# Performance work log

Measured on AMD Instinct MI355X. Metric: run time of the kernel, lower is better.

## Reference

```python
import jax, jax.numpy as jnp
import numpy as np
from jax.scipy.special import logsumexp

DIM_N, DIM_E, DIM_U = 64, 128, 64
MID, A = 32, 16
N_PER, B = 12, 128  # 128 fully-connected graphs of 12 nodes


def _lin_params(k, fin, fout):
    k1, k2 = jax.random.split(k)
    lim = 1.0 / np.sqrt(fin)
    W = jax.random.uniform(k1, (fin, fout), minval=-lim, maxval=lim)
    b = jax.random.uniform(k2, (fout,), minval=-lim, maxval=lim)
    return W, b


def setup_inputs() -> dict:
    key = jax.random.key(0)
    ks = jax.random.split(key, 12)
    # fully connected directed graph (no self loops), per component
    s, d = np.meshgrid(np.arange(N_PER), np.arange(N_PER), indexing='ij')
    m = s != d
    s1, d1 = s[m].astype(np.int64), d[m].astype(np.int64)
    Epg = s1.size  # 132
    M = np.zeros((N_PER, N_PER), np.int64)
    M[s1, d1] = np.arange(Epg)
    rev1 = M[d1, s1]
    noff = (np.arange(B, dtype=np.int64) * N_PER)[:, None]
    eoff = (np.arange(B, dtype=np.int64) * Epg)[:, None]
    src = jnp.asarray((s1[None] + noff).reshape(-1))
    dst = jnp.asarray((d1[None] + noff).reshape(-1))
    idx_revs = jnp.asarray((rev1[None] + eoff).reshape(-1))
    E, Nt = B * Epg, B * N_PER
    edge_feats = jax.random.normal(ks[0], (E, DIM_E))
    node_feats = jax.random.normal(ks[1], (Nt, DIM_N))
    graph_feats = jax.random.normal(ks[2], (B, DIM_U))
    edge_feat_reflected = edge_feats[idx_revs]
    u = jax.random.uniform(ks[3], (E, 2), minval=1e-6, maxval=1.0)
    gumbel_noise = -jnp.log(-jnp.log(u))
    W_jf, b_jf = _lin_params(ks[4], DIM_E + DIM_U, A * MID)
    W_if, b_if = _lin_params(ks[5], DIM_N + DIM_U, A)
    W_ju, b_ju = _lin_params(ks[6], DIM_E + DIM_U, A * MID)
    W_iu, b_iu = _lin_params(ks[7], DIM_N + DIM_U, A)
    W_fl, b_fl = _lin_params(ks[8], DIM_E + DIM_U, MID)
    W_cls, b_cls = _lin_params(ks[9], MID, 2)
    return dict(edge_feats=edge_feats, node_feats=node_feats, graph_feats=graph_feats,
                edge_feat_reflected=edge_feat_reflected, src=src, dst=dst, idx_revs=idx_revs,
                gumbel_noise=gumbel_noise, W_jf=W_jf, b_jf=b_jf, W_if=W_if, b_if=b_if,
                W_ju=W_ju, b_ju=b_ju, W_iu=W_iu, b_iu=b_iu, W_fl=W_fl, b_fl=b_fl,
                W_cls=W_cls, b_cls=b_cls)


def reference(edge_feats, node_feats, graph_feats, edge_feat_reflected, src, dst, idx_revs,
              gumbel_noise, W_jf, b_jf, W_if, b_if, W_ju, b_ju, W_iu, b_iu,
              W_fl, b_fl, W_cls, b_cls):
    Bn = graph_feats.shape[0]
    Nt = node_feats.shape[0]
    E = edge_feats.shape[0]
    npg = Nt // Bn          # nodes per graph == number of BP iterations
    epg = E // Bn
    a = b_if.shape[0]       # num_acts
    mid = W_cls.shape[0]    # mid_pair

    # broadcast graph-level features to edges / nodes
    u_e = jnp.repeat(graph_feats, epg, axis=0)   # [E, du]
    u_n = jnp.repeat(graph_feats, npg, axis=0)   # [Nt, du]

    xe = jnp.concatenate([edge_feats, u_e], axis=-1)
    xer = jnp.concatenate([edge_feat_reflected, u_e], axis=-1)
    xn = jnp.concatenate([node_feats, u_n], axis=-1)

    indiv_factor = xn @ W_if + b_if      # [Nt, A]
    indiv_util = xn @ W_iu + b_iu        # [Nt, A]

    fc = (xe @ W_jf + b_jf).reshape(E, a, mid)
    fcr = (xer @ W_jf + b_jf).reshape(E, a, mid)
    factor_vals = jnp.einsum('eam,ebm->eab', fc, fcr)   # [E, A, A]
    uc = (xe @ W_ju + b_ju).reshape(E, a, mid)
    ucr = (xer @ W_ju + b_ju).reshape(E, a, mid)
    util_vals = jnp.einsum('eam,ebm->eab', uc, ucr)     # [E, A, A]

    # hard gumbel-softmax edge gating; noise shared with reverse edge
    flag_repr = (xe @ W_fl + b_fl) * (xer @ W_fl + b_fl)
    logits = flag_repr @ W_cls + b_cls                  # [E, 2]
    eid = jnp.arange(E)
    noise = gumbel_noise[jnp.minimum(eid, idx_revs)]
    y_soft = jax.nn.softmax(logits + noise, axis=-1)
    y_hard = jax.nn.one_hot(jnp.argmax(y_soft, axis=-1), 2, dtype=y_soft.dtype)
    flags = y_soft + jax.lax.stop_gradient(y_hard - y_soft)
    flag0 = flags[:, 0][:, None]                        # [E, 1]

    fvT = factor_vals.transpose(0, 2, 1)
    uvT = util_vals.transpose(0, 2, 1)
    if_src, if_dst = indiv_factor[src], indiv_factor[dst]
    iu_src, iu_dst = indiv_util[src], indiv_util[dst]

    def step(carry, _):
        mm_n, um_n, msg_e, rmsg_e, umsg_e, rumsg_e = carry
        agg = mm_n[src] - rmsg_e + if_src                      # [E, A]
        m = factor_vals + agg[:, None, :]                      # [E, A, A]
        m_sum = jax.nn.log_softmax(logsumexp(m, axis=-1), axis=-1)
        new_msg = m_sum * flag0
        agg_rev = mm_n[dst] - msg_e + if_dst
        m_rev = fvT + agg_rev[:, None, :]
        m_rev_sum = jax.nn.log_softmax(logsumexp(m_rev, axis=-1), axis=-1)
        new_rmsg = m_rev_sum * flag0
        util = um_n[src] - rumsg_e + iu_src
        new_umsg = ((util_vals + util[:, None, :]) * jax.nn.softmax(m, axis=-1)).sum(-1) * flag0
        rev_util = um_n[dst] - umsg_e + iu_dst
        new_rumsg = ((uvT + rev_util[:, None, :]) * jax.nn.softmax(m_rev, axis=-1)).sum(-1) * flag0
        new_mm_n = jax.ops.segment_sum(new_msg, dst, num_segments=Nt)
        new_um_n = jax.ops.segment_sum(new_umsg, dst, num_segments=Nt)
        return (new_mm_n, new_um_n, new_msg, new_rmsg, new_umsg, new_rumsg), None

    zn = jnp.zeros((Nt, a), edge_feats.dtype)
    ze = jnp.zeros((E, a), edge_feats.dtype)
    carry0 = (zn, zn, ze, ze, ze, ze)
    (mm_n, um_n, _, _, _, _), _ = jax.lax.scan(step, carry0, None, length=npg)

    node0 = jnp.arange(Bn) * npg
    return (um_n + indiv_util)[node0]   # [B, A]
```

## Files before the change

kernel.cpp:

```cpp
#include <hip/hip_runtime.h>
#include <hip/hip_bf16.h>

typedef unsigned short ushort_t;
typedef __bf16 bf16x8 __attribute__((ext_vector_type(8)));
typedef float f32x4 __attribute__((ext_vector_type(4)));

#define E_TOT 16896
#define NT    1536
#define BGR   128
#define NPG   12
#define EPG   132
#define KD    192
#define KDE   128
#define KD2   384
#define NJ    512
#define NCAN  8448

#if defined(__has_builtin)
#  if __has_builtin(__builtin_amdgcn_global_load_lds)
#    define HAS_GLL 1
#  else
#    define HAS_GLL 0
#  endif
#else
#  define HAS_GLL 0
#endif

#if HAS_GLL
__device__ __forceinline__ void gll16(const ushort_t* g, ushort_t* s) {
    __builtin_amdgcn_global_load_lds(
        (const __attribute__((address_space(1))) unsigned int*)g,
        (__attribute__((address_space(3))) unsigned int*)s, 16, 0, 0);
}
#endif

__device__ __forceinline__ float b2f(ushort_t u) {
    union { float f; unsigned int i; } c; c.i = ((unsigned int)u) << 16; return c.f;
}
__device__ __forceinline__ ushort_t f2b(float f) {
    union { float f; unsigned int i; } c; c.f = f;
    unsigned int i = c.i;
    unsigned int r = (i + 0x7FFFu + ((i >> 16) & 1u)) >> 16;
    return (ushort_t)r;
}
__device__ __forceinline__ int rev_local(int i) {
    int s = i / 11;
    int p = i - 11 * s;
    int d = p + (p >= s ? 1 : 0);
    return d * 11 + (s < d ? s : s - 1);
}

__global__ __launch_bounds__(256) void prep_kernel(
    const float* __restrict__ Wjf, const float* __restrict__ Wju,
    const float* __restrict__ ef,  const float* __restrict__ gf,
    const float* __restrict__ bjf, const float* __restrict__ bju,
    const float* __restrict__ nf,
    const float* __restrict__ Wif, const float* __restrict__ bif,
    const float* __restrict__ Wiu, const float* __restrict__ biu,
    ushort_t* __restrict__ WtJFs, ushort_t* __restrict__ WtJUs,
    ushort_t* __restrict__ XeS, float* __restrict__ CG,
    float* __restrict__ IFF, float* __restrict__ IUU)
{
    __shared__ union {
        float tile[64][65];
        struct { float Ws[128 * 32]; float xr[8][128]; } nd;
    } sm;
    int tid = threadIdx.x;
    unsigned bx = blockIdx.x;

    if (bx < 32u) {
        int mat = bx >> 4, t16 = bx & 15;
        int k0 = (t16 >> 3) * 64, n0 = (t16 & 7) * 64;
        const float* W = mat ? Wju : Wjf;
        ushort_t* Wt = mat ? WtJUs : WtJFs;
        int col = tid & 63, rowq = tid >> 6;
#pragma unroll
        for (int i = 0; i < 16; ++i) {
            int kk = i * 4 + rowq;
            sm.tile[kk][col] = W[(size_t)(k0 + kk) * NJ + n0 + col];
        }
        __syncthreads();
        int k = tid & 63;
#pragma unroll
        for (int i = 0; i < 16; ++i) {
            int nn = i * 4 + rowq;
            float wf = sm.tile[k][nn];
            ushort_t hf = f2b(wf);
            ushort_t lo = f2b(wf - b2f(hf));
            ushort_t* dst = Wt + (size_t)(n0 + nn) * KD2 + k0 + k;
            dst[0]   = hf;
            dst[128] = hf;
            dst[256] = lo;
        }
        return;
    }
    if (bx < 1088u) {
        int t = (int)(bx - 32u) * 256 + tid;
        int e = t >> 4, k8 = t & 15;
        const float* src = ef + (size_t)e * KDE + k8 * 8;
        float4 v0 = *(const float4*)(src);
        float4 v1 = *(const float4*)(src + 4);
        float x[8] = { v0.x, v0.y, v0.z, v0.w, v1.x, v1.y, v1.z, v1.w };
        union { ushort_t u[8]; uint4 v; } hi, lo;
#pragma unroll
        for (int i = 0; i < 8; ++i) {
            ushort_t h = f2b(x[i]);
            hi.u[i] = h;
            lo.u[i] = f2b(x[i] - b2f(h));
        }
        ushort_t* dst = XeS + (size_t)e * KD2 + k8 * 8;
        *(uint4*)(dst)       = hi.v;
        *(uint4*)(dst + 128) = lo.v;
        *(uint4*)(dst + 256) = hi.v;
        return;
    }
    if (bx < 1600u) {
        int cidx = (int)(bx - 1088u) * 256 + tid;
        int z = cidx >> 16;
        int rem = cidx & 65535;
        int g = rem >> 9, n = rem & 511;
        const float* W = z ? Wju : Wjf;
        float acc = (z ? bju : bjf)[n];
        const float* gr = gf + g * 64;
#pragma unroll 8
        for (int k = 0; k < 64; ++k)
            acc += gr[k] * W[(size_t)(KDE + k) * NJ + n];
        CG[cidx] = acc;
        return;
    }
    int n0 = (int)(bx - 1600u) * 8;
    for (int i = tid; i < 128 * 32; i += 256) {
        int k = i >> 5, j = i & 31;
        sm.nd.Ws[i] = (j < 16) ? Wif[k * 16 + j] : Wiu[k * 16 + (j - 16)];
    }
    for (int i = tid; i < 8 * 128; i += 256) {
        int slot = i >> 7, k = i & 127;
        int n = n0 + slot;
        sm.nd.xr[slot][k] = (k < 64) ? nf[(size_t)n * 64 + k]
                                     : gf[(n / NPG) * 64 + (k - 64)];
    }
    __syncthreads();
    int slot = tid >> 5, j = tid & 31;
    float acc = (j < 16) ? bif[j] : biu[j - 16];
#pragma unroll 8
    for (int k = 0; k < 128; ++k) acc += sm.nd.xr[slot][k] * sm.nd.Ws[k * 32 + j];
    int n = n0 + slot;
    if (j < 16) IFF[n * 16 + j] = acc;
    else        IUU[n * 16 + (j - 16)] = acc;
}

__global__ __launch_bounds__(256) void gemm_kernel(
    const ushort_t* __restrict__ X,
    const ushort_t* __restrict__ Wt0, const ushort_t* __restrict__ Wt1,
    const float* __restrict__ CG, float* __restrict__ Hbase)
{
    __shared__ ushort_t As[2][128][32];
    __shared__ ushort_t Bs[2][128][32];
    int z = blockIdx.z;
    const ushort_t* Wt = z ? Wt1 : Wt0;
    const float* cgz = CG + (size_t)z * 128 * NJ;
    float* H = Hbase + (size_t)z * E_TOT * NJ;

    int tid = threadIdx.x, lane = tid & 63, w = tid >> 6;
    int m0 = blockIdx.y * 128, n0 = blockIdx.x * 128;
    int wm = (w >> 1) * 64, wn = (w & 1) * 64;
    int r = lane & 15, q = lane >> 4;
    f32x4 acc[4][4] = {};

    int sr = w * 32 + (lane >> 2);
    int sc = (lane & 3) * 8;
    const ushort_t* xg0 = X  + (size_t)(m0 + sr)      * KD2 + sc;
    const ushort_t* xg1 = X  + (size_t)(m0 + sr + 16) * KD2 + sc;
    const ushort_t* wg0 = Wt + (size_t)(n0 + sr)      * KD2 + sc;
    const ushort_t* wg1 = Wt + (size_t)(n0 + sr + 16) * KD2 + sc;

#if HAS_GLL
    auto stage = [&](int p, int kk) {
        gll16(xg0 + kk, &As[p][w * 32][0]);
        gll16(xg1 + kk, &As[p][w * 32 + 16][0]);
        gll16(wg0 + kk, &Bs[p][w * 32][0]);
        gll16(wg1 + kk, &Bs[p][w * 32 + 16][0]);
    };
#else
    auto stage = [&](int p, int kk) {
        uint4 a0 = *(const uint4*)(xg0 + kk);
        uint4 a1 = *(const uint4*)(xg1 + kk);
        uint4 b0 = *(const uint4*)(wg0 + kk);
        uint4 b1 = *(const uint4*)(wg1 + kk);
        *(uint4*)&As[p][sr][sc]      = a0;
        *(uint4*)&As[p][sr + 16][sc] = a1;
        *(uint4*)&Bs[p][sr][sc]      = b0;
        *(uint4*)&Bs[p][sr + 16][sc] = b1;
    };
#endif

    stage(0, 0);
    int cur = 0;
    for (int kk = 0; kk < KD2; kk += 32) {
        __syncthreads();
        if (kk + 32 < KD2) stage(cur ^ 1, kk + 32);
        bf16x8 af[4], bf[4];
#pragma unroll
        for (int mi = 0; mi < 4; ++mi)
            af[mi] = *(const bf16x8*)&As[cur][wm + mi * 16 + r][q * 8];
#pragma unroll
        for (int ni = 0; ni < 4; ++ni)
            bf[ni] = *(const bf16x8*)&Bs[cur][wn + ni * 16 + r][q * 8];
#pragma unroll
        for (int mi = 0; mi < 4; ++mi)
#pragma unroll
            for (int ni = 0; ni < 4; ++ni)
                acc[mi][ni] = __builtin_amdgcn_mfma_f32_16x16x32_bf16(
                    af[mi], bf[ni], acc[mi][ni], 0, 0, 0);
        cur ^= 1;
    }
#pragma unroll
    for (int ni = 0; ni < 4; ++ni) {
        int col = n0 + wn + ni * 16 + r;
#pragma unroll
        for (int mi = 0; mi < 4; ++mi) {
            int rowb = m0 + wm + mi * 16 + q * 4;
            float* dst = H + (size_t)rowb * NJ + col;
#pragma unroll
            for (int rr = 0; rr < 4; ++rr) {
                int gg = (rowb + rr) / EPG;
                dst[(size_t)rr * NJ] = acc[mi][ni][rr] + cgz[(size_t)gg * NJ + col];
            }
        }
    }
}

__global__ __launch_bounds__(256) void pair_kernel(
    const float* __restrict__ Hbase, float* __restrict__ Obase)
{
    __shared__ float sA[4][16][36];
    __shared__ float sB[4][16][36];
    __shared__ float sC[4][16][20];
    const float* H = Hbase + (size_t)blockIdx.y * E_TOT * NJ;
    float* OutV = Obase + (size_t)blockIdx.y * E_TOT * 256;
    int tid = threadIdx.x, w = tid >> 6, lane = tid & 63;
    int c = blockIdx.x * 4 + w;
    int gg = c / 66, cl = c - gg * 66;
    int s = 0;
    while (cl >= 11 - s) { cl -= 11 - s; ++s; }
    int d = s + 1 + cl;
    int e  = gg * EPG + s * 11 + (d - 1);
    int re = gg * EPG + d * 11 + s;
    const float* hA = H + (size_t)e * NJ;
    const float* hB = H + (size_t)re * NJ;
    int a = lane >> 2, mseg = (lane & 3) * 8;
    float4 va0 = *(const float4*)(hA + a * 32 + mseg);
    float4 va1 = *(const float4*)(hA + a * 32 + mseg + 4);
    float4 vb0 = *(const float4*)(hB + a * 32 + mseg);
    float4 vb1 = *(const float4*)(hB + a * 32 + mseg + 4);
    *(float4*)&sA[w][a][mseg]     = va0;
    *(float4*)&sA[w][a][mseg + 4] = va1;
    *(float4*)&sB[w][a][mseg]     = vb0;
    *(float4*)&sB[w][a][mseg + 4] = vb1;
    __syncthreads();

    int b = lane & 15, a0 = (lane >> 4) * 4;
    float4 ac0 = {0,0,0,0}, ac1 = {0,0,0,0}, ac2 = {0,0,0,0}, ac3 = {0,0,0,0};
#pragma unroll
    for (int m4 = 0; m4 < 8; ++m4) {
        float4 vb = *(const float4*)&sB[w][b][m4 * 4];
        float4 x0 = *(const float4*)&sA[w][a0 + 0][m4 * 4];
        float4 x1 = *(const float4*)&sA[w][a0 + 1][m4 * 4];
        float4 x2 = *(const float4*)&sA[w][a0 + 2][m4 * 4];
        float4 x3 = *(const float4*)&sA[w][a0 + 3][m4 * 4];
        ac0.x += x0.x * vb.x; ac0.y += x0.y * vb.y; ac0.z += x0.z * vb.z; ac0.w += x0.w * vb.w;
        ac1.x += x1.x * vb.x; ac1.y += x1.y * vb.y; ac1.z += x1.z * vb.z; ac1.w += x1.w * vb.w;
        ac2.x += x2.x * vb.x; ac2.y += x2.y * vb.y; ac2.z += x2.z * vb.z; ac2.w += x2.w * vb.w;
        ac3.x += x3.x * vb.x; ac3.y += x3.y * vb.y; ac3.z += x3.z * vb.z; ac3.w += x3.w * vb.w;
    }
    float v0 = ac0.x + ac0.y + ac0.z + ac0.w;
    float v1 = ac1.x + ac1.y + ac1.z + ac1.w;
    float v2 = ac2.x + ac2.y + ac2.z + ac2.w;
    float v3 = ac3.x + ac3.y + ac3.z + ac3.w;
    float* oe = OutV + (size_t)e * 256;
    oe[(a0 + 0) * 16 + b] = v0;
    oe[(a0 + 1) * 16 + b] = v1;
    oe[(a0 + 2) * 16 + b] = v2;
    oe[(a0 + 3) * 16 + b] = v3;
    sC[w][b][a0 + 0] = v0;
    sC[w][b][a0 + 1] = v1;
    sC[w][b][a0 + 2] = v2;
    sC[w][b][a0 + 3] = v3;
    __syncthreads();
    int rr = lane >> 2, cc = (lane & 3) * 4;
    float4 t4 = { sC[w][rr][cc], sC[w][rr][cc + 1], sC[w][rr][cc + 2], sC[w][rr][cc + 3] };
    *(float4*)(OutV + (size_t)re * 256 + lane * 4) = t4;
}

__global__ __launch_bounds__(256) void hfl_kernel(
    const float* __restrict__ ef, const float* __restrict__ gf,
    const float* __restrict__ Wfl, const float* __restrict__ bfl,
    float* __restrict__ HFL)
{
    __shared__ float Ws[KD][32];
    __shared__ float xr[64][KD];
    int tid = threadIdx.x;
    int e0 = blockIdx.x * 64;
    for (int i = tid; i < KD * 32; i += 256) Ws[i >> 5][i & 31] = Wfl[i];
    for (int i4 = tid; i4 < 64 * 48; i4 += 256) {
        int slot = i4 / 48, kq = i4 - slot * 48;
        int e = e0 + slot;
        float4 v;
        if (kq < 32) v = *(const float4*)&ef[(size_t)e * 128 + kq * 4];
        else         v = *(const float4*)&gf[(e / EPG) * 64 + (kq - 32) * 4];
        *(float4*)&xr[slot][kq * 4] = v;
    }
    __syncthreads();
    int j = tid & 31, es = tid >> 5;
    float acc[8];
#pragma unroll
    for (int i = 0; i < 8; ++i) acc[i] = bfl[j];
    for (int k = 0; k < KD; k += 4) {
        float w0 = Ws[k][j], w1 = Ws[k + 1][j], w2 = Ws[k + 2][j], w3 = Ws[k + 3][j];
#pragma unroll
        for (int i = 0; i < 8; ++i) {
            float4 x4 = *(const float4*)&xr[es + 8 * i][k];
            acc[i] += x4.x * w0; acc[i] += x4.y * w1;
            acc[i] += x4.z * w2; acc[i] += x4.w * w3;
        }
    }
#pragma unroll
    for (int i = 0; i < 8; ++i)
        HFL[(size_t)(e0 + es + 8 * i) * 32 + j] = acc[i];
}

__global__ __launch_bounds__(704, 3) void bp_kernel(
    const float* __restrict__ FV, const float* __restrict__ UV,
    const float* __restrict__ HFL, const float* __restrict__ Wcls,
    const float* __restrict__ bcls, const float* __restrict__ gum,
    const float* __restrict__ IFF, const float* __restrict__ IUU,
    float* __restrict__ out)
{
    int g = blockIdx.x, tid = threadIdx.x;
    __shared__ float msg[2][EPG][16];
    __shared__ float umsg[2][EPG][16];
    __shared__ float Asum[NPG][16], Usum[NPG][16];
    __shared__ float iffs[NPG][16], iuus[NPG][16];
    __shared__ float fls[EPG];

    for (int i = tid; i < 2 * EPG * 16; i += 704) {
        (&msg[0][0][0])[i] = 0.f;
        (&umsg[0][0][0])[i] = 0.f;
    }
    if (tid < NPG * 16) {
        float fi = IFF[g * NPG * 16 + tid];
        float ui = IUU[g * NPG * 16 + tid];
        (&iffs[0][0])[tid] = fi; (&iuus[0][0])[tid] = ui;
        (&Asum[0][0])[tid] = fi; (&Usum[0][0])[tid] = ui;
    }
    if (tid < EPG) {
        int el = tid, rel = rev_local(el);
        int e = g * EPG + el, re = g * EPG + rel;
        float l0 = bcls[0], l1 = bcls[1];
        const float* ha = HFL + (size_t)e * 32;
        const float* hb = HFL + (size_t)re * 32;
#pragma unroll
        for (int j = 0; j < 32; ++j) {
            float pp = ha[j] * hb[j];
            l0 += pp * Wcls[j * 2 + 0];
            l1 += pp * Wcls[j * 2 + 1];
        }
        int mn = min(e, re);
        l0 += gum[(size_t)mn * 2 + 0];
        l1 += gum[(size_t)mn * 2 + 1];
        fls[el] = (l0 >= l1) ? 1.0f : 0.0f;
    }

    int w44 = tid >> 4, a = tid & 15;
    int sidx[3], ridx[3], eidx[3];
    float fv[3][16], uv[3][16], fle[3];
    const float* fvg = FV + (size_t)g * EPG * 256;
    const float* uvg = UV + (size_t)g * EPG * 256;
#pragma unroll
    for (int j = 0; j < 3; ++j) {
        int e = j * 44 + w44;
        eidx[j] = e;
        sidx[j] = e / 11;
        ridx[j] = rev_local(e);
        const float* fr = fvg + (size_t)e * 256 + a * 16;
        const float* ur = uvg + (size_t)e * 256 + a * 16;
#pragma unroll
        for (int qq = 0; qq < 4; ++qq) {
            float4 f4 = *(const float4*)(fr + qq * 4);
            float4 u4 = *(const float4*)(ur + qq * 4);
            fv[j][qq * 4 + 0] = f4.x; fv[j][qq * 4 + 1] = f4.y;
            fv[j][qq * 4 + 2] = f4.z; fv[j][qq * 4 + 3] = f4.w;
            uv[j][qq * 4 + 0] = u4.x; uv[j][qq * 4 + 1] = u4.y;
            uv[j][qq * 4 + 2] = u4.z; uv[j][qq * 4 + 3] = u4.w;
        }
    }
    __syncthreads();
#pragma unroll
    for (int j = 0; j < 3; ++j) fle[j] = fls[eidx[j]];

    int cur = 0;
    for (int it = 0; it < NPG; ++it) {
        int nxt = cur ^ 1;
#pragma unroll
        for (int j = 0; j < 3; ++j) {
            int e = eidx[j], s = sidx[j], re = ridx[j];
            float t_m[16], t_u[16];
#pragma unroll
            for (int qq = 0; qq < 4; ++qq) {
                float4 av  = *(const float4*)&Asum[s][qq * 4];
                float4 mv  = *(const float4*)&msg[cur][re][qq * 4];
                float4 usv = *(const float4*)&Usum[s][qq * 4];
                float4 umv = *(const float4*)&umsg[cur][re][qq * 4];
                t_m[qq * 4 + 0] = fv[j][qq * 4 + 0] + (av.x - mv.x);
                t_m[qq * 4 + 1] = fv[j][qq * 4 + 1] + (av.y - mv.y);
                t_m[qq * 4 + 2] = fv[j][qq * 4 + 2] + (av.z - mv.z);
                t_m[qq * 4 + 3] = fv[j][qq * 4 + 3] + (av.w - mv.w);
                t_u[qq * 4 + 0] = uv[j][qq * 4 + 0] + (usv.x - umv.x);
                t_u[qq * 4 + 1] = uv[j][qq * 4 + 1] + (usv.y - umv.y);
                t_u[qq * 4 + 2] = uv[j][qq * 4 + 2] + (usv.z - umv.z);
                t_u[qq * 4 + 3] = uv[j][qq * 4 + 3] + (usv.w - umv.w);
            }
            float mx = t_m[0];
#pragma unroll
            for (int b = 1; b < 16; ++b) mx = fmaxf(mx, t_m[b]);
            float S = 0.f, num = 0.f;
#pragma unroll
            for (int b = 0; b < 16; ++b) {
                float ev = __expf(t_m[b] - mx);
                S += ev;
                num += t_u[b] * ev;
            }
            float lse = mx + __logf(S);
            float unv = num / S;
            float M2 = lse;
            M2 = fmaxf(M2, __shfl_xor(M2, 1));
            M2 = fmaxf(M2, __shfl_xor(M2, 2));
            M2 = fmaxf(M2, __shfl_xor(M2, 4));
            M2 = fmaxf(M2, __shfl_xor(M2, 8));
            float se = __expf(lse - M2);
            se += __shfl_xor(se, 1);
            se += __shfl_xor(se, 2);
            se += __shfl_xor(se, 4);
            se += __shfl_xor(se, 8);
            float LSE = M2 + __logf(se);
            msg[nxt][e][a] = (lse - LSE) * fle[j];
            umsg[nxt][e][a] = unv * fle[j];
        }
        __syncthreads();
        if (tid < NPG * 16) {
            int n = tid >> 4, aa = tid & 15;
            float sm = 0.f, su = 0.f;
#pragma unroll
            for (int s = 0; s < NPG; ++s) {
                if (s == n) continue;
                int le = s * 11 + (n < s ? n : n - 1);
                sm += msg[nxt][le][aa];
                su += umsg[nxt][le][aa];
            }
            Asum[n][aa] = sm + iffs[n][aa];
            Usum[n][aa] = su + iuus[n][aa];
        }
        __syncthreads();
        cur = nxt;
    }
    if (tid < 16) {
        out[g * 16 + tid] = Usum[0][tid];
    }
}

extern "C" void kernel_launch(void* const* d_in, const int* in_sizes, int n_in,
                              void* d_out, int out_size, void* d_ws, size_t ws_size,
                              hipStream_t stream) {
    const float* edge_feats  = (const float*)d_in[0];
    const float* node_feats  = (const float*)d_in[1];
    const float* graph_feats = (const float*)d_in[2];
    const float* gumbel      = (const float*)d_in[7];
    const float* W_jf        = (const float*)d_in[8];
    const float* b_jf        = (const float*)d_in[9];
    const float* W_if        = (const float*)d_in[10];
    const float* b_if        = (const float*)d_in[11];
    const float* W_ju        = (const float*)d_in[12];
    const float* b_ju        = (const float*)d_in[13];
    const float* W_iu        = (const float*)d_in[14];
    const float* b_iu        = (const float*)d_in[15];
    const float* W_fl        = (const float*)d_in[16];
    const float* b_fl        = (const float*)d_in[17];
    const float* W_cls       = (const float*)d_in[18];
    const float* b_cls       = (const float*)d_in[19];
    float* out = (float*)d_out;
    (void)in_sizes; (void)n_in; (void)out_size; (void)ws_size;

    size_t off = 0;
    char* base = (char*)d_ws;
    auto alloc = [&](size_t bytes) {
        void* p = base + off;
        off += (bytes + 255) & ~(size_t)255;
        return p;
    };
    ushort_t* XeS   = (ushort_t*)alloc((size_t)E_TOT * KD2 * 2);
    ushort_t* WtJFs = (ushort_t*)alloc((size_t)NJ * KD2 * 2);
    ushort_t* WtJUs = (ushort_t*)alloc((size_t)NJ * KD2 * 2);
    float*    CGp   = (float*)   alloc((size_t)2 * 128 * NJ * 4);
    float*    HFL   = (float*)   alloc((size_t)E_TOT * 32 * 4);
    float*    IFFp  = (float*)   alloc((size_t)NT * 16 * 4);
    float*    IUUp  = (float*)   alloc((size_t)NT * 16 * 4);
    float*    H2    = (float*)   alloc((size_t)E_TOT * NJ * 2 * 4);
    float*    FVUV  = (float*)   alloc((size_t)E_TOT * 512 * 4);
    float* FVv = FVUV;
    float* UVv = FVUV + (size_t)E_TOT * 256;

    const int prep_blocks = 32 + 1056 + 512 + 192;

    prep_kernel<<<prep_blocks, 256, 0, stream>>>(
        W_jf, W_ju, edge_feats, graph_feats, b_jf, b_ju, node_feats,
        W_if, b_if, W_iu, b_iu, WtJFs, WtJUs, XeS, CGp, IFFp, IUUp);
    hfl_kernel<<<E_TOT / 64, 256, 0, stream>>>(edge_feats, graph_feats, W_fl, b_fl, HFL);
    gemm_kernel<<<dim3(NJ / 128, E_TOT / 128, 2), 256, 0, stream>>>(
        XeS, WtJFs, WtJUs, CGp, H2);
    pair_kernel<<<dim3(NCAN / 4, 2), 256, 0, stream>>>(H2, FVUV);
    bp_kernel<<<BGR, 704, 0, stream>>>(FVv, UVv, HFL, W_cls, b_cls, gumbel,
                                       IFFp, IUUp, out);
}
```

Before: 233.1 us.

## Unroll BP edge work into pinned registers and trim final iteration to node-0 edges

The per-thread FV/UV rows of the belief-propagation kernel are loaded into named float4 registers, and empty asm constraints pin them so the compiler keeps them resident. The three edge computations are interleaved before their shuffle-based normalisations to expose more instruction-level parallelism. The last of the 12 iterations now computes only the utility messages on edges into node 0, since only those feed the output, and sums them directly. Launch attributes now fix waves-per-EU at 3, and the LDS array is padded with a large unused buffer, apparently to cap occupancy. The padding and the register pinning add LDS and register pressure for an unclear benefit.

Measured after the change: 257.0 us. +10.2%, slower.

```diff
diff --git a/kernel.cpp b/kernel.cpp
--- a/kernel.cpp
+++ b/kernel.cpp
@@ -329,7 +329,10 @@
         HFL[(size_t)(e0 + es + 8 * i) * 32 + j] = acc[i];
 }
 
-__global__ __launch_bounds__(704, 3) void bp_kernel(
+__global__ void
+__attribute__((amdgpu_flat_work_group_size(704, 704)))
+__attribute__((amdgpu_waves_per_eu(3, 3)))
+bp_kernel(
     const float* __restrict__ FV, const float* __restrict__ UV,
     const float* __restrict__ HFL, const float* __restrict__ Wcls,
     const float* __restrict__ bcls, const float* __restrict__ gum,
@@ -341,7 +344,7 @@
     __shared__ float umsg[2][EPG][16];
     __shared__ float Asum[NPG][16], Usum[NPG][16];
     __shared__ float iffs[NPG][16], iuus[NPG][16];
-    __shared__ float fls[EPG];
+    __shared__ float fls[EPG + 11200];
 
     for (int i = tid; i < 2 * EPG * 16; i += 704) {
         (&msg[0][0][0])[i] = 0.f;
@@ -372,80 +375,148 @@
     }
 
     int w44 = tid >> 4, a = tid & 15;
-    int sidx[3], ridx[3], eidx[3];
-    float fv[3][16], uv[3][16], fle[3];
     const float* fvg = FV + (size_t)g * EPG * 256;
     const float* uvg = UV + (size_t)g * EPG * 256;
-#pragma unroll
-    for (int j = 0; j < 3; ++j) {
-        int e = j * 44 + w44;
-        eidx[j] = e;
-        sidx[j] = e / 11;
-        ridx[j] = rev_local(e);
-        const float* fr = fvg + (size_t)e * 256 + a * 16;
-        const float* ur = uvg + (size_t)e * 256 + a * 16;
-#pragma unroll
-        for (int qq = 0; qq < 4; ++qq) {
-            float4 f4 = *(const float4*)(fr + qq * 4);
-            float4 u4 = *(const float4*)(ur + qq * 4);
-            fv[j][qq * 4 + 0] = f4.x; fv[j][qq * 4 + 1] = f4.y;
-            fv[j][qq * 4 + 2] = f4.z; fv[j][qq * 4 + 3] = f4.w;
-            uv[j][qq * 4 + 0] = u4.x; uv[j][qq * 4 + 1] = u4.y;
-            uv[j][qq * 4 + 2] = u4.z; uv[j][qq * 4 + 3] = u4.w;
-        }
-    }
+
+    int e0 = w44,      s0 = e0 / 11, r0 = rev_local(e0);
+    int e1 = 44 + w44, s1 = e1 / 11, r1 = rev_local(e1);
+    int e2 = 88 + w44, s2 = e2 / 11, r2 = rev_local(e2);
+
+    const float* fr0 = fvg + (size_t)e0 * 256 + a * 16;
+    const float* ur0 = uvg + (size_t)e0 * 256 + a * 16;
+    const float* fr1 = fvg + (size_t)e1 * 256 + a * 16;
+    const float* ur1 = uvg + (size_t)e1 * 256 + a * 16;
+    const float* fr2 = fvg + (size_t)e2 * 256 + a * 16;
+    const float* ur2 = uvg + (size_t)e2 * 256 + a * 16;
+
+    float4 f0q0 = *(const float4*)(fr0 + 0),  f0q1 = *(const float4*)(fr0 + 4);
+    float4 f0q2 = *(const float4*)(fr0 + 8),  f0q3 = *(const float4*)(fr0 + 12);
+    float4 u0q0 = *(const float4*)(ur0 + 0),  u0q1 = *(const float4*)(ur0 + 4);
+    float4 u0q2 = *(const float4*)(ur0 + 8),  u0q3 = *(const float4*)(ur0 + 12);
+    float4 f1q0 = *(const float4*)(fr1 + 0),  f1q1 = *(const float4*)(fr1 + 4);
+    float4 f1q2 = *(const float4*)(fr1 + 8),  f1q3 = *(const float4*)(fr1 + 12);
+    float4 u1q0 = *(const float4*)(ur1 + 0),  u1q1 = *(const float4*)(ur1 + 4);
+    float4 u1q2 = *(const float4*)(ur1 + 8),  u1q3 = *(const float4*)(ur1 + 12);
+    float4 f2q0 = *(const float4*)(fr2 + 0),  f2q1 = *(const float4*)(fr2 + 4);
+    float4 f2q2 = *(const float4*)(fr2 + 8),  f2q3 = *(const float4*)(fr2 + 12);
+    float4 u2q0 = *(const float4*)(ur2 + 0),  u2q1 = *(const float4*)(ur2 + 4);
+    float4 u2q2 = *(const float4*)(ur2 + 8),  u2q3 = *(const float4*)(ur2 + 12);
+
+#define PIN4(v) asm volatile("" : "+v"(v.x), "+v"(v.y), "+v"(v.z), "+v"(v.w))
+    PIN4(f0q0); PIN4(f0q1); PIN4(f0q2); PIN4(f0q3);
+    PIN4(u0q0); PIN4(u0q1); PIN4(u0q2); PIN4(u0q3);
+    PIN4(f1q0); PIN4(f1q1); PIN4(f1q2); PIN4(f1q3);
+    PIN4(u1q0); PIN4(u1q1); PIN4(u1q2); PIN4(u1q3);
+    PIN4(f2q0); PIN4(f2q1); PIN4(f2q2); PIN4(f2q3);
+    PIN4(u2q0); PIN4(u2q1); PIN4(u2q2); PIN4(u2q3);
+#undef PIN4
+
     __syncthreads();
-#pragma unroll
-    for (int j = 0; j < 3; ++j) fle[j] = fls[eidx[j]];
+    float fl0 = fls[e0], fl1 = fls[e1], fl2 = fls[e2];
 
     int cur = 0;
-    for (int it = 0; it < NPG; ++it) {
+
+    auto edge_core = [&](int s, int re,
+                         float4 f0, float4 f1, float4 f2, float4 f3,
+                         float4 u0, float4 u1, float4 u2, float4 u3,
+                         float& lse_o, float& unv_o) {
+        float m0, m1, m2, m3, m4, m5, m6, m7, m8, m9, m10, m11, m12, m13, m14, m15;
+        {
+            float4 av = *(const float4*)&Asum[s][0];
+            float4 mv = *(const float4*)&msg[cur][re][0];
+            m0 = f0.x + (av.x - mv.x); m1 = f0.y + (av.y - mv.y);
+            m2 = f0.z + (av.z - mv.z); m3 = f0.w + (av.w - mv.w);
+        }
+        {
+            float4 av = *(const float4*)&Asum[s][4];
+            float4 mv = *(const float4*)&msg[cur][re][4];
+            m4 = f1.x + (av.x - mv.x); m5 = f1.y + (av.y - mv.y);
+            m6 = f1.z + (av.z - mv.z); m7 = f1.w + (av.w - mv.w);
+        }
+        {
+            float4 av = *(const float4*)&Asum[s][8];
+            float4 mv = *(const float4*)&msg[cur][re][8];
+            m8 = f2.x + (av.x - mv.x); m9 = f2.y + (av.y - mv.y);
+            m10 = f2.z + (av.z - mv.z); m11 = f2.w + (av.w - mv.w);
+        }
+        {
+            float4 av = *(const float4*)&Asum[s][12];
+            float4 mv = *(const float4*)&msg[cur][re][12];
+            m12 = f3.x + (av.x - mv.x); m13 = f3.y + (av.y - mv.y);
+            m14 = f3.z + (av.z - mv.z); m15 = f3.w + (av.w - mv.w);
+        }
+        float mx = m0;
+        mx = fmaxf(mx, m1);  mx = fmaxf(mx, m2);  mx = fmaxf(mx, m3);
+        mx = fmaxf(mx, m4);  mx = fmaxf(mx, m5);  mx = fmaxf(mx, m6);
+        mx = fmaxf(mx, m7);  mx = fmaxf(mx, m8);  mx = fmaxf(mx, m9);
+        mx = fmaxf(mx, m10); mx = fmaxf(mx, m11); mx = fmaxf(mx, m12);
+        mx = fmaxf(mx, m13); mx = fmaxf(mx, m14); mx = fmaxf(mx, m15);
+        float S = 0.f, num = 0.f;
+        {
+            float4 usv = *(const float4*)&Usum[s][0];
+            float4 umv = *(const float4*)&umsg[cur][re][0];
+            float ev, tu;
+            ev = __expf(m0 - mx); S += ev; tu = u0.x + (usv.x - umv.x); num += tu * ev;
+            ev = __expf(m1 - mx); S += ev; tu = u0.y + (usv.y - umv.y); num += tu * ev;
+            ev = __expf(m2 - mx); S += ev; tu = u0.z + (usv.z - umv.z); num += tu * ev;
+            ev = __expf(m3 - mx); S += ev; tu = u0.w + (usv.w - umv.w); num += tu * ev;
+        }
+        {
+            float4 usv = *(const float4*)&Usum[s][4];
+            float4 umv = *(const float4*)&umsg[cur][re][4];
+            float ev, tu;
+            ev = __expf(m4 - mx); S += ev; tu = u1.x + (usv.x - umv.x); num += tu * ev;
+            ev = __expf(m5 - mx); S += ev; tu = u1.y + (usv.y - umv.y); num += tu * ev;
+            ev = __expf(m6 - mx); S += ev; tu = u1.z + (usv.z - umv.z); num += tu * ev;
+            ev = __expf(m7 - mx); S += ev; tu = u1.w + (usv.w - umv.w); num += tu * ev;
+        }
+        {
+            float4 usv = *(const float4*)&Usum[s][8];
+            float4 umv = *(const float4*)&umsg[cur][re][8];
+            float ev, tu;
+            ev = __expf(m8 - mx);  S += ev; tu = u2.x + (usv.x - umv.x); num += tu * ev;
+            ev = __expf(m9 - mx);  S += ev; tu = u2.y + (usv.y - umv.y); num += tu * ev;
+            ev = __expf(m10 - mx); S += ev; tu = u2.z + (usv.z - umv.z); num += tu * ev;
+            ev = __expf(m11 - mx); S += ev; tu = u2.w + (usv.w - umv.w); num += tu * ev;
+        }
+        {
+            float4 usv = *(const float4*)&Usum[s][12];
+            float4 umv = *(const float4*)&umsg[cur][re][12];
+            float ev, tu;
+            ev = __expf(m12 - mx); S += ev; tu = u3.x + (usv.x - umv.x); num += tu * ev;
+            ev = __expf(m13 - mx); S += ev; tu = u3.y + (usv.y - umv.y); num += tu * ev;
+            ev = __expf(m14 - mx); S += ev; tu = u3.z + (usv.z - umv.z); num += tu * ev;
+            ev = __expf(m15 - mx); S += ev; tu = u3.w + (usv.w - umv.w); num += tu * ev;
+        }
+        lse_o = mx + __logf(S);
+        unv_o = num / S;
+    };
+
+    auto finish = [&](int e, float lse, float unv, float fl, int nxt) {
+        float M2 = lse;
+        M2 = fmaxf(M2, __shfl_xor(M2, 1));
+        M2 = fmaxf(M2, __shfl_xor(M2, 2));
+        M2 = fmaxf(M2, __shfl_xor(M2, 4));
+        M2 = fmaxf(M2, __shfl_xor(M2, 8));
+        float se = __expf(lse - M2);
+        se += __shfl_xor(se, 1);
+        se += __shfl_xor(se, 2);
+        se += __shfl_xor(se, 4);
+        se += __shfl_xor(se, 8);
+        float LSE = M2 + __logf(se);
+        msg[nxt][e][a] = (lse - LSE) * fl;
+        umsg[nxt][e][a] = unv * fl;
+    };
+
+    for (int it = 0; it < NPG - 1; ++it) {
         int nxt = cur ^ 1;
-#pragma unroll
-        for (int j = 0; j < 3; ++j) {
-            int e = eidx[j], s = sidx[j], re = ridx[j];
-            float t_m[16], t_u[16];
-#pragma unroll
-            for (int qq = 0; qq < 4; ++qq) {
-                float4 av  = *(const float4*)&Asum[s][qq * 4];
-                float4 mv  = *(const float4*)&msg[cur][re][qq * 4];
-                float4 usv = *(const float4*)&Usum[s][qq * 4];
-                float4 umv = *(const float4*)&umsg[cur][re][qq * 4];
-                t_m[qq * 4 + 0] = fv[j][qq * 4 + 0] + (av.x - mv.x);
-                t_m[qq * 4 + 1] = fv[j][qq * 4 + 1] + (av.y - mv.y);
-                t_m[qq * 4 + 2] = fv[j][qq * 4 + 2] + (av.z - mv.z);
-                t_m[qq * 4 + 3] = fv[j][qq * 4 + 3] + (av.w - mv.w);
-                t_u[qq * 4 + 0] = uv[j][qq * 4 + 0] + (usv.x - umv.x);
-                t_u[qq * 4 + 1] = uv[j][qq * 4 + 1] + (usv.y - umv.y);
-                t_u[qq * 4 + 2] = uv[j][qq * 4 + 2] + (usv.z - umv.z);
-                t_u[qq * 4 + 3] = uv[j][qq * 4 + 3] + (usv.w - umv.w);
-            }
-            float mx = t_m[0];
-#pragma unroll
-            for (int b = 1; b < 16; ++b) mx = fmaxf(mx, t_m[b]);
-            float S = 0.f, num = 0.f;
-#pragma unroll
-            for (int b = 0; b < 16; ++b) {
-                float ev = __expf(t_m[b] - mx);
-                S += ev;
-                num += t_u[b] * ev;
-            }
-            float lse = mx + __logf(S);
-            float unv = num / S;
-            float M2 = lse;
-            M2 = fmaxf(M2, __shfl_xor(M2, 1));
-            M2 = fmaxf(M2, __shfl_xor(M2, 2));
-            M2 = fmaxf(M2, __shfl_xor(M2, 4));
-            M2 = fmaxf(M2, __shfl_xor(M2, 8));
-            float se = __expf(lse - M2);
-            se += __shfl_xor(se, 1);
-            se += __shfl_xor(se, 2);
-            se += __shfl_xor(se, 4);
-            se += __shfl_xor(se, 8);
-            float LSE = M2 + __logf(se);
-            msg[nxt][e][a] = (lse - LSE) * fle[j];
-            umsg[nxt][e][a] = unv * fle[j];
-        }
+        float lse0, unv0, lse1, unv1, lse2, unv2;
+        edge_core(s0, r0, f0q0, f0q1, f0q2, f0q3, u0q0, u0q1, u0q2, u0q3, lse0, unv0);
+        edge_core(s1, r1, f1q0, f1q1, f1q2, f1q3, u1q0, u1q1, u1q2, u1q3, lse1, unv1);
+        edge_core(s2, r2, f2q0, f2q1, f2q2, f2q3, u2q0, u2q1, u2q2, u2q3, lse2, unv2);
+        finish(e0, lse0, unv0, fl0, nxt);
+        finish(e1, lse1, unv1, fl1, nxt);
+        finish(e2, lse2, unv2, fl2, nxt);
         __syncthreads();
         if (tid < NPG * 16) {
             int n = tid >> 4, aa = tid & 15;
@@ -463,8 +534,27 @@
         __syncthreads();
         cur = nxt;
     }
-    if (tid < 16) {
-        out[g * 16 + tid] = Usum[0][tid];
+
+    {
+        int nxt = cur ^ 1;
+        if ((w44 % 11) == 0) {
+            float lse, unv;
+            if (e0 != 0) {
+                edge_core(s0, r0, f0q0, f0q1, f0q2, f0q3, u0q0, u0q1, u0q2, u0q3, lse, unv);
+                umsg[nxt][e0][a] = unv * fl0;
+            }
+            edge_core(s1, r1, f1q0, f1q1, f1q2, f1q3, u1q0, u1q1, u1q2, u1q3, lse, unv);
+            umsg[nxt][e1][a] = unv * fl1;
+            edge_core(s2, r2, f2q0, f2q1, f2q2, f2q3, u2q0, u2q1, u2q2, u2q3, lse, unv);
+            umsg[nxt][e2][a] = unv * fl2;
+        }
+        __syncthreads();
+        if (tid < 16) {
+            float su = 0.f;
+#pragma unroll
+            for (int s = 1; s < NPG; ++s) su += umsg[nxt][s * 11][tid];
+            out[g * 16 + tid] = su + iuus[0][tid];
+        }
     }
 }
 
```
